# Kernel optimization log

Measured on AMD Instinct MI355X. Metric: run time of the kernel, lower is better.

The kernel has to match this reference:

```python
import jax, jax.numpy as jnp
import numpy as np

TEMPERATURE = 4.0

def setup_inputs() -> dict:
    key = jax.random.key(0)
    k1, k2 = jax.random.split(key)
    query = jax.random.normal(k1, (128, 128, 256), dtype=jnp.float32)      # (B, D, Q)
    context = jax.random.normal(k2, (128, 128, 32, 32), dtype=jnp.float32)  # (B, D, H, W)
    return {"query": query, "context": context}

def reference(query, context):
    B, D, Q = query.shape
    H, W = context.shape[2], context.shape[3]
    L = H * W  # context_length
    context_flat = context.reshape(B, D, L)                    # (B, D, L)
    # scores[b, l, q] = sum_d context[b, d, l] * query[b, d, q]
    scores = jnp.einsum('bdl,bdq->blq', context_flat, query)   # (B, L, Q)
    # first softmax: over query dim (context -> query)
    attn_q = jax.nn.softmax(scores, axis=-1)                   # (B, L, Q)
    # second softmax: over context dim with temperature (query -> context)
    attn_c = jax.nn.softmax(attn_q.transpose(0, 2, 1) * TEMPERATURE, axis=-1)  # (B, Q, L)
    # weighted_context[b, d, q] = sum_l context[b, d, l] * attn_c[b, q, l]
    weighted_context = jnp.einsum('bdl,bql->bdq', context_flat, attn_c)  # (B, D, Q)
    attention_map = attn_c.reshape(B, Q, H, W)
    return (weighted_context, attention_map)
```

## Files before the change

### kernel.cpp

```cpp
#include <hip/hip_runtime.h>
#include <math.h>

#define B_ 128
#define D_ 128
#define Q_ 256
#define L_ 1024

typedef __attribute__((ext_vector_type(8))) short s16x8;
typedef __attribute__((ext_vector_type(4))) float f32x4;
typedef unsigned short u16;

__device__ __forceinline__ u16 f2bf(float x) {
  unsigned u = __float_as_uint(x);
  u += 0x7FFF + ((u >> 16) & 1);
  return (u16)(u >> 16);
}
__device__ __forceinline__ float bf2f(u16 h) {
  return __uint_as_float(((unsigned)h) << 16);
}
__device__ __forceinline__ uint2 pack4bf(float4 v) {
  uint2 r;
  r.x = ((unsigned)f2bf(v.y) << 16) | (unsigned)f2bf(v.x);
  r.y = ((unsigned)f2bf(v.w) << 16) | (unsigned)f2bf(v.z);
  return r;
}
__device__ __forceinline__ void split8(const float* x, s16x8& hi, s16x8& lo) {
#pragma unroll
  for (int j = 0; j < 8; j++) {
    u16 h = f2bf(x[j]);
    hi[j] = (short)h;
    lo[j] = (short)f2bf(x[j] - bf2f(h));
  }
}

__global__ __launch_bounds__(256) void k0_split(const float* __restrict__ query,
                                                u16* __restrict__ qhi,
                                                u16* __restrict__ qlo) {
  __shared__ float sm0[128][65];
  const int b = blockIdx.y, q0 = blockIdx.x * 64;
  const int tid = threadIdx.x;
  {
    const int dr = tid >> 4;
    const int lc = (tid & 15) * 4;
#pragma unroll
    for (int h = 0; h < 8; h++) {
      const int d = h * 16 + dr;
      float4 v = *(const float4*)(query + ((size_t)b * D_ + d) * Q_ + q0 + lc);
      sm0[d][lc] = v.x;
      sm0[d][lc + 1] = v.y;
      sm0[d][lc + 2] = v.z;
      sm0[d][lc + 3] = v.w;
    }
  }
  __syncthreads();
  const int qr = tid >> 2;
  const int dc = (tid & 3) * 32;
  u16* ph = qhi + ((size_t)b * Q_ + q0 + qr) * D_ + dc;
  u16* pl = qlo + ((size_t)b * Q_ + q0 + qr) * D_ + dc;
#pragma unroll
  for (int c = 0; c < 4; c++) {
    s16x8 hv, lv;
#pragma unroll
    for (int j = 0; j < 8; j++) {
      float x = sm0[dc + c * 8 + j][qr];
      u16 h = f2bf(x);
      hv[j] = (short)h;
      lv[j] = (short)f2bf(x - bf2f(h));
    }
    *(s16x8*)(ph + c * 8) = hv;
    *(s16x8*)(pl + c * 8) = lv;
  }
}

__global__ __launch_bounds__(256, 3) void k1_attnq(
    const u16* __restrict__ qhi, const u16* __restrict__ qlo,
    const float* __restrict__ ctx, float* __restrict__ attq,
    float* __restrict__ pd) {
  __shared__ u16 CsH[64][48], CsL[64][48];
  __shared__ float sm[4][64], ss[4][64], fm[64], fs[64];
  const int lt = blockIdx.x, b = blockIdx.y;
  const int l0 = lt * 64;
  const int tid = threadIdx.x;
  const int wq = tid >> 6;
  const int lane = tid & 63, quad = lane >> 4, l15 = lane & 15;

  const float* Cb = ctx + (size_t)b * D_ * L_ + l0;
  const u16* Qh = qhi + ((size_t)b * Q_ + wq * 64 + l15) * D_;
  const u16* Ql = qlo + ((size_t)b * Q_ + wq * 64 + l15) * D_;

  const int dd = tid >> 3;
  const int lc = (tid & 7) * 8;

  f32x4 acc[4][4];
#pragma unroll
  for (int mi = 0; mi < 4; mi++)
#pragma unroll
    for (int ni = 0; ni < 4; ni++) acc[mi][ni] = (f32x4){0.f, 0.f, 0.f, 0.f};

#pragma unroll 2
  for (int k0 = 0; k0 < D_; k0 += 32) {
    if (k0) __syncthreads();
    const float* cp = Cb + (size_t)(k0 + dd) * L_ + lc;
    float4 v0 = *(const float4*)cp;
    float4 v1 = *(const float4*)(cp + 4);
    float xv[8] = {v0.x, v0.y, v0.z, v0.w, v1.x, v1.y, v1.z, v1.w};
#pragma unroll
    for (int j = 0; j < 8; j++) {
      const int ll = lc + j;
      const int col = ((((dd >> 3) ^ (ll >> 3)) & 3) << 3) | (dd & 7);
      u16 h = f2bf(xv[j]);
      CsH[ll][col] = h;
      CsL[ll][col] = f2bf(xv[j] - bf2f(h));
    }
    __syncthreads();

    s16x8 bh[4], bl[4];
#pragma unroll
    for (int ni = 0; ni < 4; ni++) {
      const int ll = ni * 16 + l15;
      const int cc = ((quad ^ (ll >> 3)) & 3) << 3;
      bh[ni] = *(const s16x8*)&CsH[ll][cc];
      bl[ni] = *(const s16x8*)&CsL[ll][cc];
    }
#pragma unroll
    for (int mi = 0; mi < 4; mi++) {
      const s16x8 ah =
          *(const s16x8*)(Qh + (size_t)mi * 16 * D_ + k0 + quad * 8);
      const s16x8 al =
          *(const s16x8*)(Ql + (size_t)mi * 16 * D_ + k0 + quad * 8);
#pragma unroll
      for (int ni = 0; ni < 4; ni++) {
        acc[mi][ni] = __builtin_amdgcn_mfma_f32_16x16x32_bf16(
            ah, bh[ni], acc[mi][ni], 0, 0, 0);
        acc[mi][ni] = __builtin_amdgcn_mfma_f32_16x16x32_bf16(
            ah, bl[ni], acc[mi][ni], 0, 0, 0);
        acc[mi][ni] = __builtin_amdgcn_mfma_f32_16x16x32_bf16(
            al, bh[ni], acc[mi][ni], 0, 0, 0);
      }
    }
  }

#pragma unroll
  for (int ni = 0; ni < 4; ni++) {
    float m = -1e30f;
#pragma unroll
    for (int mi = 0; mi < 4; mi++)
#pragma unroll
      for (int r = 0; r < 4; r++) m = fmaxf(m, acc[mi][ni][r]);
    m = fmaxf(m, __shfl_xor(m, 16));
    m = fmaxf(m, __shfl_xor(m, 32));
    float s = 0.f;
#pragma unroll
    for (int mi = 0; mi < 4; mi++)
#pragma unroll
      for (int r = 0; r < 4; r++) s += __expf(acc[mi][ni][r] - m);
    s += __shfl_xor(s, 16);
    s += __shfl_xor(s, 32);
    if (quad == 0) {
      sm[wq][ni * 16 + l15] = m;
      ss[wq][ni * 16 + l15] = s;
    }
  }
  __syncthreads();
  if (tid < 64) {
    float m0 = sm[0][tid], m1 = sm[1][tid], m2 = sm[2][tid], m3 = sm[3][tid];
    float M = fmaxf(fmaxf(m0, m1), fmaxf(m2, m3));
    float S = ss[0][tid] * __expf(m0 - M) + ss[1][tid] * __expf(m1 - M) +
              ss[2][tid] * __expf(m2 - M) + ss[3][tid] * __expf(m3 - M);
    fm[tid] = M;
    fs[tid] = 1.f / S;
  }
  __syncthreads();

  float fmv[4], fiv[4];
#pragma unroll
  for (int ni = 0; ni < 4; ni++) {
    fmv[ni] = fm[ni * 16 + l15];
    fiv[ni] = fs[ni * 16 + l15];
  }
  float* Ab = attq + ((size_t)b * Q_ + wq * 64) * L_ + l0;
  float dsum[4][4];
#pragma unroll
  for (int mi = 0; mi < 4; mi++)
#pragma unroll
    for (int r = 0; r < 4; r++) dsum[mi][r] = 0.f;
#pragma unroll
  for (int mi = 0; mi < 4; mi++)
#pragma unroll
    for (int r = 0; r < 4; r++) {
      const int q = mi * 16 + quad * 4 + r;
#pragma unroll
      for (int ni = 0; ni < 4; ni++) {
        float a = __expf(acc[mi][ni][r] - fmv[ni]) * fiv[ni];
        Ab[(size_t)q * L_ + ni * 16 + l15] = a;
        dsum[mi][r] += __expf(4.f * a);
      }
    }
#pragma unroll
  for (int mi = 0; mi < 4; mi++)
#pragma unroll
    for (int r = 0; r < 4; r++) {
      float v = dsum[mi][r];
      v += __shfl_xor(v, 1);
      v += __shfl_xor(v, 2);
      v += __shfl_xor(v, 4);
      v += __shfl_xor(v, 8);
      dsum[mi][r] = v;
    }
  if (l15 == 0) {
#pragma unroll
    for (int mi = 0; mi < 4; mi++)
#pragma unroll
      for (int r = 0; r < 4; r++)
        pd[(size_t)lt * (B_ * Q_) + b * Q_ + wq * 64 + mi * 16 + quad * 4 +
           r] = dsum[mi][r];
  }
}

__global__ __launch_bounds__(256, 2) void k1_attnq_legacy(
    const float* __restrict__ query, const float* __restrict__ ctx,
    float* __restrict__ attq, float* __restrict__ pd) {
  __shared__ float sm[4][64], ss[4][64], fm[64], fs[64];
  const int lt = blockIdx.x, b = blockIdx.y;
  const int l0 = lt * 64;
  const int tid = threadIdx.x;
  const int wq = tid >> 6;
  const int lane = tid & 63, quad = lane >> 4, l15 = lane & 15;

  const float* Qb = query + (size_t)b * D_ * Q_;
  const float* Cb = ctx + (size_t)b * D_ * L_ + l0;

  f32x4 acc[4][4];
#pragma unroll
  for (int mi = 0; mi < 4; mi++)
#pragma unroll
    for (int ni = 0; ni < 4; ni++) acc[mi][ni] = (f32x4){0.f, 0.f, 0.f, 0.f};

#pragma unroll 2
  for (int k0 = 0; k0 < D_; k0 += 32) {
    const int kq = k0 + quad * 8;
    s16x8 ah[4], al[4], bh[4], bl[4];
#pragma unroll
    for (int mi = 0; mi < 4; mi++) {
      const float* p = Qb + (size_t)kq * Q_ + wq * 64 + mi * 16 + l15;
      float x[8];
#pragma unroll
      for (int j = 0; j < 8; j++) x[j] = p[(size_t)j * Q_];
      split8(x, ah[mi], al[mi]);
    }
#pragma unroll
    for (int ni = 0; ni < 4; ni++) {
      const float* p = Cb + (size_t)kq * L_ + ni * 16 + l15;
      float x[8];
#pragma unroll
      for (int j = 0; j < 8; j++) x[j] = p[(size_t)j * L_];
      split8(x, bh[ni], bl[ni]);
    }
#pragma unroll
    for (int mi = 0; mi < 4; mi++)
#pragma unroll
      for (int ni = 0; ni < 4; ni++) {
        acc[mi][ni] = __builtin_amdgcn_mfma_f32_16x16x32_bf16(
            ah[mi], bh[ni], acc[mi][ni], 0, 0, 0);
        acc[mi][ni] = __builtin_amdgcn_mfma_f32_16x16x32_bf16(
            ah[mi], bl[ni], acc[mi][ni], 0, 0, 0);
        acc[mi][ni] = __builtin_amdgcn_mfma_f32_16x16x32_bf16(
            al[mi], bh[ni], acc[mi][ni], 0, 0, 0);
      }
  }

#pragma unroll
  for (int ni = 0; ni < 4; ni++) {
    float m = -1e30f;
#pragma unroll
    for (int mi = 0; mi < 4; mi++)
#pragma unroll
      for (int r = 0; r < 4; r++) m = fmaxf(m, acc[mi][ni][r]);
    m = fmaxf(m, __shfl_xor(m, 16));
    m = fmaxf(m, __shfl_xor(m, 32));
    float s = 0.f;
#pragma unroll
    for (int mi = 0; mi < 4; mi++)
#pragma unroll
      for (int r = 0; r < 4; r++) s += __expf(acc[mi][ni][r] - m);
    s += __shfl_xor(s, 16);
    s += __shfl_xor(s, 32);
    if (quad == 0) {
      sm[wq][ni * 16 + l15] = m;
      ss[wq][ni * 16 + l15] = s;
    }
  }
  __syncthreads();
  if (tid < 64) {
    float m0 = sm[0][tid], m1 = sm[1][tid], m2 = sm[2][tid], m3 = sm[3][tid];
    float M = fmaxf(fmaxf(m0, m1), fmaxf(m2, m3));
    float S = ss[0][tid] * __expf(m0 - M) + ss[1][tid] * __expf(m1 - M) +
              ss[2][tid] * __expf(m2 - M) + ss[3][tid] * __expf(m3 - M);
    fm[tid] = M;
    fs[tid] = 1.f / S;
  }
  __syncthreads();

  float fmv[4], fiv[4];
#pragma unroll
  for (int ni = 0; ni < 4; ni++) {
    fmv[ni] = fm[ni * 16 + l15];
    fiv[ni] = fs[ni * 16 + l15];
  }
  float* Ab = attq + ((size_t)b * Q_ + wq * 64) * L_ + l0;
  float dsum[4][4];
#pragma unroll
  for (int mi = 0; mi < 4; mi++)
#pragma unroll
    for (int r = 0; r < 4; r++) dsum[mi][r] = 0.f;
#pragma unroll
  for (int mi = 0; mi < 4; mi++)
#pragma unroll
    for (int r = 0; r < 4; r++) {
      const int q = mi * 16 + quad * 4 + r;
#pragma unroll
      for (int ni = 0; ni < 4; ni++) {
        float a = __expf(acc[mi][ni][r] - fmv[ni]) * fiv[ni];
        Ab[(size_t)q * L_ + ni * 16 + l15] = a;
        dsum[mi][r] += __expf(4.f * a);
      }
    }
#pragma unroll
  for (int mi = 0; mi < 4; mi++)
#pragma unroll
    for (int r = 0; r < 4; r++) {
      float v = dsum[mi][r];
      v += __shfl_xor(v, 1);
      v += __shfl_xor(v, 2);
      v += __shfl_xor(v, 4);
      v += __shfl_xor(v, 8);
      dsum[mi][r] = v;
    }
  if (l15 == 0) {
#pragma unroll
    for (int mi = 0; mi < 4; mi++)
#pragma unroll
      for (int r = 0; r < 4; r++)
        pd[(size_t)lt * (B_ * Q_) + b * Q_ + wq * 64 + mi * 16 + quad * 4 +
           r] = dsum[mi][r];
  }
}

__global__ __launch_bounds__(256) void k2_invd(const float* __restrict__ pd,
                                               float* __restrict__ invd) {
  const int i = blockIdx.x * 256 + threadIdx.x;
  float s = 0.f;
#pragma unroll
  for (int t = 0; t < 16; t++) s += pd[(size_t)t * (B_ * Q_) + i];
  invd[i] = 1.f / s;
}

__global__ __launch_bounds__(256) void k4_weighted(
    const float* __restrict__ ctx, float* __restrict__ attn,
    const float* __restrict__ invd, float* __restrict__ W) {
  __shared__ unsigned short As[128][32];
  __shared__ unsigned short Bs[64][32];
  const int b = blockIdx.y, q0 = blockIdx.x * 64;
  const int tid = threadIdx.x;
  const int w = tid >> 6, lane = tid & 63, quad = lane >> 4, l15 = lane & 15;
  const int wd = (w >> 1) * 64, wn = (w & 1) * 32;

  const float* Cb = ctx + (size_t)b * D_ * L_;
  float* Ab = attn + ((size_t)b * Q_ + q0) * L_;

  const int lc = (tid & 7) * 4;
  const int rr = tid >> 3;
  const float id0 = invd[b * Q_ + q0 + rr];
  const float id1 = invd[b * Q_ + q0 + rr + 32];

  f32x4 acc[4][2];
#pragma unroll
  for (int mi = 0; mi < 4; mi++)
#pragma unroll
    for (int ni = 0; ni < 2; ni++) acc[mi][ni] = (f32x4){0.f, 0.f, 0.f, 0.f};

  for (int l0 = 0; l0 < L_; l0 += 32) {
    if (l0) __syncthreads();
#pragma unroll
    for (int h = 0; h < 4; h++) {
      const int d = rr + h * 32;
      float4 cv = *(const float4*)(Cb + (size_t)d * L_ + l0 + lc);
      *(uint2*)&As[d][lc] = pack4bf(cv);
    }
#pragma unroll
    for (int h = 0; h < 2; h++) {
      const int q = rr + h * 32;
      float* p = Ab + (size_t)q * L_ + l0 + lc;
      float4 a = *(const float4*)p;
      const float idv = h ? id1 : id0;
      float4 t;
      t.x = __expf(4.f * a.x) * idv;
      t.y = __expf(4.f * a.y) * idv;
      t.z = __expf(4.f * a.z) * idv;
      t.w = __expf(4.f * a.w) * idv;
      *(float4*)p = t;
      *(uint2*)&Bs[q][lc] = pack4bf(t);
    }
    __syncthreads();

    s16x8 af[4], bq[2];
#pragma unroll
    for (int mi = 0; mi < 4; mi++)
      af[mi] = *(const s16x8*)&As[wd + mi * 16 + l15][quad * 8];
#pragma unroll
    for (int ni = 0; ni < 2; ni++)
      bq[ni] = *(const s16x8*)&Bs[wn + ni * 16 + l15][quad * 8];
#pragma unroll
    for (int mi = 0; mi < 4; mi++)
#pragma unroll
      for (int ni = 0; ni < 2; ni++)
        acc[mi][ni] = __builtin_amdgcn_mfma_f32_16x16x32_bf16(
            af[mi], bq[ni], acc[mi][ni], 0, 0, 0);
  }

  float* Wb = W + (size_t)b * D_ * Q_;
#pragma unroll
  for (int mi = 0; mi < 4; mi++)
#pragma unroll
    for (int ni = 0; ni < 2; ni++)
#pragma unroll
      for (int r = 0; r < 4; r++)
        Wb[(size_t)(wd + mi * 16 + quad * 4 + r) * Q_ + q0 + wn + ni * 16 +
           l15] = acc[mi][ni][r];
}

extern "C" void kernel_launch(void* const* d_in, const int* in_sizes, int n_in,
                              void* d_out, int out_size, void* d_ws,
                              size_t ws_size, hipStream_t stream) {
  const float* query = (const float*)d_in[0];
  const float* ctx = (const float*)d_in[1];
  float* W = (float*)d_out;
  float* attn = (float*)d_out + (size_t)B_ * D_ * Q_;

  const size_t nQT = (size_t)B_ * Q_ * D_;
  const size_t need_pd = (size_t)17 * B_ * Q_ * sizeof(float);
  const size_t need_full = nQT * 2 * sizeof(u16) + need_pd;

  if (d_ws && ws_size >= need_full) {
    u16* qh = (u16*)d_ws;
    u16* ql = qh + nQT;
    float* pd = (float*)(ql + nQT);
    float* invd = pd + (size_t)16 * B_ * Q_;
    k0_split<<<dim3(Q_ / 64, B_), 256, 0, stream>>>(query, qh, ql);
    k1_attnq<<<dim3(L_ / 64, B_), 256, 0, stream>>>(qh, ql, ctx, attn, pd);
    k2_invd<<<dim3(B_ * Q_ / 256), 256, 0, stream>>>(pd, invd);
    k4_weighted<<<dim3(Q_ / 64, B_), 256, 0, stream>>>(ctx, attn, invd, W);
  } else {
    float* pd = (d_ws && ws_size >= need_pd) ? (float*)d_ws : W;
    float* invd = pd + (size_t)16 * B_ * Q_;
    k1_attnq_legacy<<<dim3(L_ / 64, B_), 256, 0, stream>>>(query, ctx, attn,
                                                           pd);
    k2_invd<<<dim3(B_ * Q_ / 256), 256, 0, stream>>>(pd, invd);
    k4_weighted<<<dim3(Q_ / 64, B_), 256, 0, stream>>>(ctx, attn, invd, W);
  }
}
```

Baseline: 332.9 us.

## Recompute scores in fused kernel instead of storing attn_q intermediate

```diff
diff --git a/kernel.cpp b/kernel.cpp
--- a/kernel.cpp
+++ b/kernel.cpp
@@ -33,50 +33,9 @@
   }
 }
 
-__global__ __launch_bounds__(256) void k0_split(const float* __restrict__ query,
-                                                u16* __restrict__ qhi,
-                                                u16* __restrict__ qlo) {
-  __shared__ float sm0[128][65];
-  const int b = blockIdx.y, q0 = blockIdx.x * 64;
-  const int tid = threadIdx.x;
-  {
-    const int dr = tid >> 4;
-    const int lc = (tid & 15) * 4;
-#pragma unroll
-    for (int h = 0; h < 8; h++) {
-      const int d = h * 16 + dr;
-      float4 v = *(const float4*)(query + ((size_t)b * D_ + d) * Q_ + q0 + lc);
-      sm0[d][lc] = v.x;
-      sm0[d][lc + 1] = v.y;
-      sm0[d][lc + 2] = v.z;
-      sm0[d][lc + 3] = v.w;
-    }
-  }
-  __syncthreads();
-  const int qr = tid >> 2;
-  const int dc = (tid & 3) * 32;
-  u16* ph = qhi + ((size_t)b * Q_ + q0 + qr) * D_ + dc;
-  u16* pl = qlo + ((size_t)b * Q_ + q0 + qr) * D_ + dc;
-#pragma unroll
-  for (int c = 0; c < 4; c++) {
-    s16x8 hv, lv;
-#pragma unroll
-    for (int j = 0; j < 8; j++) {
-      float x = sm0[dc + c * 8 + j][qr];
-      u16 h = f2bf(x);
-      hv[j] = (short)h;
-      lv[j] = (short)f2bf(x - bf2f(h));
-    }
-    *(s16x8*)(ph + c * 8) = hv;
-    *(s16x8*)(pl + c * 8) = lv;
-  }
-}
-
-__global__ __launch_bounds__(256, 3) void k1_attnq(
-    const u16* __restrict__ qhi, const u16* __restrict__ qlo,
-    const float* __restrict__ ctx, float* __restrict__ attq,
-    float* __restrict__ pd) {
-  __shared__ u16 CsH[64][48], CsL[64][48];
+__global__ __launch_bounds__(256, 2) void k1_stats(
+    const float* __restrict__ query, const float* __restrict__ ctx,
+    float* __restrict__ pd, float* __restrict__ fmg, float* __restrict__ fsg) {
   __shared__ float sm[4][64], ss[4][64], fm[64], fs[64];
   const int lt = blockIdx.x, b = blockIdx.y;
   const int l0 = lt * 64;
@@ -84,12 +43,8 @@
   const int wq = tid >> 6;
   const int lane = tid & 63, quad = lane >> 4, l15 = lane & 15;
 
+  const float* Qb = query + (size_t)b * D_ * Q_;
   const float* Cb = ctx + (size_t)b * D_ * L_ + l0;
-  const u16* Qh = qhi + ((size_t)b * Q_ + wq * 64 + l15) * D_;
-  const u16* Ql = qlo + ((size_t)b * Q_ + wq * 64 + l15) * D_;
-
-  const int dd = tid >> 3;
-  const int lc = (tid & 7) * 8;
 
   f32x4 acc[4][4];
 #pragma unroll
@@ -99,45 +54,35 @@
 
 #pragma unroll 2
   for (int k0 = 0; k0 < D_; k0 += 32) {
-    if (k0) __syncthreads();
-    const float* cp = Cb + (size_t)(k0 + dd) * L_ + lc;
-    float4 v0 = *(const float4*)cp;
-    float4 v1 = *(const float4*)(cp + 4);
-    float xv[8] = {v0.x, v0.y, v0.z, v0.w, v1.x, v1.y, v1.z, v1.w};
-#pragma unroll
-    for (int j = 0; j < 8; j++) {
-      const int ll = lc + j;
-      const int col = ((((dd >> 3) ^ (ll >> 3)) & 3) << 3) | (dd & 7);
-      u16 h = f2bf(xv[j]);
-      CsH[ll][col] = h;
-      CsL[ll][col] = f2bf(xv[j] - bf2f(h));
-    }
-    __syncthreads();
-
-    s16x8 bh[4], bl[4];
+    const int kq = k0 + quad * 8;
+    s16x8 ah[4], al[4], bh[4], bl[4];
+#pragma unroll
+    for (int mi = 0; mi < 4; mi++) {
+      const float* p = Qb + (size_t)kq * Q_ + wq * 64 + mi * 16 + l15;
+      float x[8];
+#pragma unroll
+      for (int j = 0; j < 8; j++) x[j] = p[(size_t)j * Q_];
+      split8(x, ah[mi], al[mi]);
+    }
 #pragma unroll
     for (int ni = 0; ni < 4; ni++) {
-      const int ll = ni * 16 + l15;
-      const int cc = ((quad ^ (ll >> 3)) & 3) << 3;
-      bh[ni] = *(const s16x8*)&CsH[ll][cc];
-      bl[ni] = *(const s16x8*)&CsL[ll][cc];
-    }
-#pragma unroll
-    for (int mi = 0; mi < 4; mi++) {
-      const s16x8 ah =
-          *(const s16x8*)(Qh + (size_t)mi * 16 * D_ + k0 + quad * 8);
-      const s16x8 al =
-          *(const s16x8*)(Ql + (size_t)mi * 16 * D_ + k0 + quad * 8);
+      const float* p = Cb + (size_t)kq * L_ + ni * 16 + l15;
+      float x[8];
+#pragma unroll
+      for (int j = 0; j < 8; j++) x[j] = p[(size_t)j * L_];
+      split8(x, bh[ni], bl[ni]);
+    }
+#pragma unroll
+    for (int mi = 0; mi < 4; mi++)
 #pragma unroll
       for (int ni = 0; ni < 4; ni++) {
         acc[mi][ni] = __builtin_amdgcn_mfma_f32_16x16x32_bf16(
-            ah, bh[ni], acc[mi][ni], 0, 0, 0);
-        acc[mi][ni] = __builtin_amdgcn_mfma_f32_16x16x32_bf16(
-            ah, bl[ni], acc[mi][ni], 0, 0, 0);
-        acc[mi][ni] = __builtin_amdgcn_mfma_f32_16x16x32_bf16(
-            al, bh[ni], acc[mi][ni], 0, 0, 0);
-      }
-    }
+            ah[mi], bh[ni], acc[mi][ni], 0, 0, 0);
+        acc[mi][ni] = __builtin_amdgcn_mfma_f32_16x16x32_bf16(
+            ah[mi], bl[ni], acc[mi][ni], 0, 0, 0);
+        acc[mi][ni] = __builtin_amdgcn_mfma_f32_16x16x32_bf16(
+            al[mi], bh[ni], acc[mi][ni], 0, 0, 0);
+      }
   }
 
 #pragma unroll
@@ -169,6 +114,8 @@
               ss[2][tid] * __expf(m2 - M) + ss[3][tid] * __expf(m3 - M);
     fm[tid] = M;
     fs[tid] = 1.f / S;
+    fmg[(size_t)b * L_ + l0 + tid] = M;
+    fsg[(size_t)b * L_ + l0 + tid] = 1.f / S;
   }
   __syncthreads();
 
@@ -178,7 +125,6 @@
     fmv[ni] = fm[ni * 16 + l15];
     fiv[ni] = fs[ni * 16 + l15];
   }
-  float* Ab = attq + ((size_t)b * Q_ + wq * 64) * L_ + l0;
   float dsum[4][4];
 #pragma unroll
   for (int mi = 0; mi < 4; mi++)
@@ -188,11 +134,9 @@
   for (int mi = 0; mi < 4; mi++)
 #pragma unroll
     for (int r = 0; r < 4; r++) {
-      const int q = mi * 16 + quad * 4 + r;
 #pragma unroll
       for (int ni = 0; ni < 4; ni++) {
         float a = __expf(acc[mi][ni][r] - fmv[ni]) * fiv[ni];
-        Ab[(size_t)q * L_ + ni * 16 + l15] = a;
         dsum[mi][r] += __expf(4.f * a);
       }
     }
@@ -215,6 +159,144 @@
         pd[(size_t)lt * (B_ * Q_) + b * Q_ + wq * 64 + mi * 16 + quad * 4 +
            r] = dsum[mi][r];
   }
+}
+
+__global__ __launch_bounds__(256, 2) void k3_fused(
+    const float* __restrict__ query, const float* __restrict__ ctx,
+    const float* __restrict__ pd, const float* __restrict__ fmg,
+    const float* __restrict__ fsg, float* __restrict__ attn,
+    float* __restrict__ W) {
+  __shared__ u16 QsH[64][136], QsL[64][136];
+  __shared__ u16 As[128][72];
+  __shared__ u16 Bs[64][72];
+  __shared__ float ivs[64];
+  const int b = blockIdx.y, q0 = blockIdx.x * 64;
+  const int tid = threadIdx.x;
+  const int w = tid >> 6, lane = tid & 63, quad = lane >> 4, l15 = lane & 15;
+
+  if (tid < 64) {
+    float s = 0.f;
+#pragma unroll
+    for (int t = 0; t < 16; t++)
+      s += pd[(size_t)t * (B_ * Q_) + b * Q_ + q0 + tid];
+    ivs[tid] = 1.f / s;
+  }
+  {
+    const int dr = tid >> 1;
+    const int qc = (tid & 1) * 32;
+    const float* qp = query + ((size_t)b * D_ + dr) * Q_ + q0 + qc;
+#pragma unroll
+    for (int c = 0; c < 8; c++) {
+      float4 v = *(const float4*)(qp + c * 4);
+      float xs[4] = {v.x, v.y, v.z, v.w};
+#pragma unroll
+      for (int j = 0; j < 4; j++) {
+        u16 h = f2bf(xs[j]);
+        QsH[qc + c * 4 + j][dr] = h;
+        QsL[qc + c * 4 + j][dr] = f2bf(xs[j] - bf2f(h));
+      }
+    }
+  }
+  __syncthreads();
+
+  float ivq[4];
+#pragma unroll
+  for (int ni = 0; ni < 4; ni++) ivq[ni] = ivs[ni * 16 + l15];
+  const int wd = (w >> 1) * 64, wn = (w & 1) * 32;
+  f32x4 accw[4][2];
+#pragma unroll
+  for (int mi = 0; mi < 4; mi++)
+#pragma unroll
+    for (int ni = 0; ni < 2; ni++) accw[mi][ni] = (f32x4){0.f, 0.f, 0.f, 0.f};
+
+  const float* Cb = ctx + (size_t)b * D_ * L_;
+  float* Mapb = attn + ((size_t)b * Q_ + q0) * L_;
+  const float* fmb = fmg + (size_t)b * L_;
+  const float* fsb = fsg + (size_t)b * L_;
+  const int dd = tid >> 3;
+  const int lc8 = (tid & 7) * 8;
+
+  for (int l0 = 0; l0 < L_; l0 += 64) {
+    if (l0) __syncthreads();
+#pragma unroll
+    for (int h = 0; h < 4; h++) {
+      const int d = dd + h * 32;
+      const float* cp = Cb + (size_t)d * L_ + l0 + lc8;
+      float4 v0 = *(const float4*)cp;
+      float4 v1 = *(const float4*)(cp + 4);
+      *(uint2*)&As[d][lc8] = pack4bf(v0);
+      *(uint2*)&As[d][lc8 + 4] = pack4bf(v1);
+    }
+
+    f32x4 accs[4];
+#pragma unroll
+    for (int ni = 0; ni < 4; ni++) accs[ni] = (f32x4){0.f, 0.f, 0.f, 0.f};
+#pragma unroll
+    for (int ks = 0; ks < 4; ks++) {
+      const float* ap =
+          Cb + (size_t)(ks * 32 + quad * 8) * L_ + l0 + 16 * w + l15;
+      float x[8];
+#pragma unroll
+      for (int j = 0; j < 8; j++) x[j] = ap[(size_t)j * L_];
+      s16x8 ch, cl;
+      split8(x, ch, cl);
+#pragma unroll
+      for (int ni = 0; ni < 4; ni++) {
+        const s16x8 qh = *(const s16x8*)&QsH[ni * 16 + l15][ks * 32 + quad * 8];
+        const s16x8 ql = *(const s16x8*)&QsL[ni * 16 + l15][ks * 32 + quad * 8];
+        accs[ni] =
+            __builtin_amdgcn_mfma_f32_16x16x32_bf16(ch, qh, accs[ni], 0, 0, 0);
+        accs[ni] =
+            __builtin_amdgcn_mfma_f32_16x16x32_bf16(ch, ql, accs[ni], 0, 0, 0);
+        accs[ni] =
+            __builtin_amdgcn_mfma_f32_16x16x32_bf16(cl, qh, accs[ni], 0, 0, 0);
+      }
+    }
+
+    float fml[4], fsl[4];
+#pragma unroll
+    for (int r = 0; r < 4; r++) {
+      fml[r] = fmb[l0 + 16 * w + quad * 4 + r];
+      fsl[r] = fsb[l0 + 16 * w + quad * 4 + r];
+    }
+#pragma unroll
+    for (int ni = 0; ni < 4; ni++)
+#pragma unroll
+      for (int r = 0; r < 4; r++) {
+        float a = __expf(accs[ni][r] - fml[r]) * fsl[r];
+        float t = __expf(4.f * a) * ivq[ni];
+        Mapb[(size_t)(ni * 16 + l15) * L_ + l0 + 16 * w + quad * 4 + r] = t;
+        Bs[ni * 16 + l15][16 * w + quad * 4 + r] = f2bf(t);
+      }
+    __syncthreads();
+
+#pragma unroll
+    for (int ks2 = 0; ks2 < 2; ks2++) {
+      s16x8 af[4], bq[2];
+#pragma unroll
+      for (int mi = 0; mi < 4; mi++)
+        af[mi] = *(const s16x8*)&As[wd + mi * 16 + l15][ks2 * 32 + quad * 8];
+#pragma unroll
+      for (int ni = 0; ni < 2; ni++)
+        bq[ni] = *(const s16x8*)&Bs[wn + ni * 16 + l15][ks2 * 32 + quad * 8];
+#pragma unroll
+      for (int mi = 0; mi < 4; mi++)
+#pragma unroll
+        for (int ni = 0; ni < 2; ni++)
+          accw[mi][ni] = __builtin_amdgcn_mfma_f32_16x16x32_bf16(
+              af[mi], bq[ni], accw[mi][ni], 0, 0, 0);
+    }
+  }
+
+  float* Wb = W + (size_t)b * D_ * Q_;
+#pragma unroll
+  for (int mi = 0; mi < 4; mi++)
+#pragma unroll
+    for (int ni = 0; ni < 2; ni++)
+#pragma unroll
+      for (int r = 0; r < 4; r++)
+        Wb[(size_t)(wd + mi * 16 + quad * 4 + r) * Q_ + q0 + wn + ni * 16 +
+           l15] = accw[mi][ni][r];
 }
 
 __global__ __launch_bounds__(256, 2) void k1_attnq_legacy(
@@ -432,25 +514,25 @@
 extern "C" void kernel_launch(void* const* d_in, const int* in_sizes, int n_in,
                               void* d_out, int out_size, void* d_ws,
                               size_t ws_size, hipStream_t stream) {
+  (void)in_sizes;
+  (void)n_in;
+  (void)out_size;
   const float* query = (const float*)d_in[0];
   const float* ctx = (const float*)d_in[1];
   float* W = (float*)d_out;
   float* attn = (float*)d_out + (size_t)B_ * D_ * Q_;
 
-  const size_t nQT = (size_t)B_ * Q_ * D_;
-  const size_t need_pd = (size_t)17 * B_ * Q_ * sizeof(float);
-  const size_t need_full = nQT * 2 * sizeof(u16) + need_pd;
-
-  if (d_ws && ws_size >= need_full) {
-    u16* qh = (u16*)d_ws;
-    u16* ql = qh + nQT;
-    float* pd = (float*)(ql + nQT);
-    float* invd = pd + (size_t)16 * B_ * Q_;
-    k0_split<<<dim3(Q_ / 64, B_), 256, 0, stream>>>(query, qh, ql);
-    k1_attnq<<<dim3(L_ / 64, B_), 256, 0, stream>>>(qh, ql, ctx, attn, pd);
-    k2_invd<<<dim3(B_ * Q_ / 256), 256, 0, stream>>>(pd, invd);
-    k4_weighted<<<dim3(Q_ / 64, B_), 256, 0, stream>>>(ctx, attn, invd, W);
+  const size_t need =
+      ((size_t)16 * B_ * Q_ + (size_t)2 * B_ * L_) * sizeof(float);
+  if (d_ws && ws_size >= need) {
+    float* pd = (float*)d_ws;
+    float* fm = pd + (size_t)16 * B_ * Q_;
+    float* fs = fm + (size_t)B_ * L_;
+    k1_stats<<<dim3(L_ / 64, B_), 256, 0, stream>>>(query, ctx, pd, fm, fs);
+    k3_fused<<<dim3(Q_ / 64, B_), 256, 0, stream>>>(query, ctx, pd, fm, fs,
+                                                    attn, W);
   } else {
+    const size_t need_pd = (size_t)17 * B_ * Q_ * sizeof(float);
     float* pd = (d_ws && ws_size >= need_pd) ? (float*)d_ws : W;
     float* invd = pd + (size_t)16 * B_ * Q_;
     k1_attnq_legacy<<<dim3(L_ / 64, B_), 256, 0, stream>>>(query, ctx, attn,
```

Measured after the change: 300.3 us. 1.11x faster.
